# Kernel tuning notes

Hardware: AMD Instinct MI355X
Metric: run time of the kernel (lower is better)

Reference implementation:

```python
import jax, jax.numpy as jnp
import numpy as np
from jax.ops import segment_sum

N_NODES = 100000
N_EDGES = 1600000
IN_DIM, HID_DIM, OUT_DIM = 64, 48, 32


def setup_inputs() -> dict:
    key = jax.random.key(0)
    ks = jax.random.split(key, 4)
    x = jax.random.normal(ks[0], (N_NODES, IN_DIM), dtype=jnp.float32)
    edge_index = jax.random.randint(ks[1], (2, N_EDGES), 0, N_NODES, dtype=jnp.int64)
    W1 = jax.random.normal(ks[2], (IN_DIM, HID_DIM), dtype=jnp.float32) / np.sqrt(IN_DIM)
    b1 = jnp.zeros((HID_DIM,), dtype=jnp.float32)
    W2 = jax.random.normal(ks[3], (HID_DIM, OUT_DIM), dtype=jnp.float32) / np.sqrt(HID_DIM)
    b2 = jnp.zeros((OUT_DIM,), dtype=jnp.float32)
    return {"x": x, "edge_index": edge_index, "W1": W1, "b1": b1, "W2": W2, "b2": b2}


def _gcn_conv(x, W, b, src, dst, deg_inv_sqrt, n_nodes):
    # GCNConv: out = D^{-1/2} (A + I) D^{-1/2} (x W) + b
    h = x @ W                                   # [N, F_out]
    norm = deg_inv_sqrt[src] * deg_inv_sqrt[dst]  # [E+N]
    msg = h[src] * norm[:, None]                # gather + scale
    out = segment_sum(msg, dst, num_segments=n_nodes)  # scatter-add over dst
    return out + b


def reference(x, edge_index, W1, b1, W2, b2):
    n = x.shape[0]
    loop = jnp.arange(n, dtype=edge_index.dtype)
    src = jnp.concatenate([edge_index[0], loop])  # add self-loops (PyG default)
    dst = jnp.concatenate([edge_index[1], loop])
    deg = segment_sum(jnp.ones_like(dst, dtype=x.dtype), dst, num_segments=n)
    deg_inv_sqrt = jnp.where(deg > 0, jax.lax.rsqrt(jnp.maximum(deg, 1.0)), 0.0)
    h = _gcn_conv(x, W1, b1, src, dst, deg_inv_sqrt, n)
    h = jax.nn.relu(h)
    embeddings = _gcn_conv(h, W2, b2, src, dst, deg_inv_sqrt, n)
    return embeddings
```

## Files before the change

### kernel.cpp

```cpp
#include <hip/hip_runtime.h>
#include <hip/hip_fp16.h>


#define NN 100000
#define NE 1600000
#define NPB 128
#define NBUCK ((NN + NPB - 1) / NPB)
#define PBITS 17
#define PMASK ((1 << PBITS) - 1)
#define CHB 3
#define CHS 14
#define NKEY (NPB << CHB)
#define PART_B 512
#define EPT 8
#define PART_G ((NE + PART_B * EPT - 1) / (PART_B * EPT))
#define CAP 4096
#define UN 8

struct alignas(8)  half4 { __half2 lo, hi; };
struct alignas(16) half8 { __half2 a, b, c, d; };

__global__ void k_part(const int* __restrict__ src, const int* __restrict__ dst,
                       int* __restrict__ cursor, int* __restrict__ packed) {
    __shared__ int h[NBUCK];
    __shared__ int base[NBUCK];
    for (int i = threadIdx.x; i < NBUCK; i += blockDim.x) h[i] = 0;
    __syncthreads();
    int ebase = blockIdx.x * (PART_B * EPT);
    for (int k = 0; k < EPT; ++k) {
        int e = ebase + k * PART_B + threadIdx.x;
        if (e < NE) atomicAdd(&h[dst[e] >> 7], 1);
    }
    __syncthreads();
    for (int i = threadIdx.x; i < NBUCK; i += blockDim.x) {
        int c = h[i];
        if (c) base[i] = atomicAdd(&cursor[i], c);
        h[i] = 0;
    }
    __syncthreads();
    for (int k = 0; k < EPT; ++k) {
        int e = ebase + k * PART_B + threadIdx.x;
        if (e < NE) {
            int d = dst[e];
            int b = d >> 7;
            int r = atomicAdd(&h[b], 1);
            packed[(size_t)b * CAP + base[b] + r] = src[e] | ((d & (NPB - 1)) << PBITS);
        }
    }
}

__global__ void k_bsort(const int* __restrict__ packed, const int* __restrict__ cursor,
                        int* __restrict__ srcsort, unsigned int* __restrict__ rowinfo,
                        float* __restrict__ dinv) {
    __shared__ int stage[CAP];
    __shared__ int cnt[NKEY];
    __shared__ int tsum[256];
    int tid = threadIdx.x, b = blockIdx.x;
    int e0 = b * CAP, sz = cursor[b];
    for (int i = tid; i < NKEY; i += 256) cnt[i] = 0;
    __syncthreads();
    for (int i = tid; i < sz; i += 256) {
        int w = packed[e0 + i];
        stage[i] = w;
        int key = ((w >> PBITS) << CHB) | ((w & PMASK) >> CHS);
        atomicAdd(&cnt[key], 1);
    }
    __syncthreads();
    int k0 = tid * 4;
    int c0 = cnt[k0], c1 = cnt[k0 + 1], c2 = cnt[k0 + 2], c3 = cnt[k0 + 3];
    int loc = c0 + c1 + c2 + c3;
    tsum[tid] = loc;
    __syncthreads();
    for (int off = 1; off < 256; off <<= 1) {
        int v = (tid >= off) ? tsum[tid - off] : 0;
        __syncthreads();
        tsum[tid] += v;
        __syncthreads();
    }
    int base = tsum[tid] - loc;
    cnt[k0]     = base;
    cnt[k0 + 1] = base + c0;
    cnt[k0 + 2] = base + c0 + c1;
    cnt[k0 + 3] = base + c0 + c1 + c2;
    __syncthreads();
    if (tid < NPB) {
        int node = b * NPB + tid;
        int rs = cnt[tid << CHB];
        int re = (tid == NPB - 1) ? sz : cnt[(tid + 1) << CHB];
        if (node < NN) {
            rowinfo[node] = ((unsigned int)(e0 + rs) << 10) | (unsigned int)(re - rs);
            dinv[node] = rsqrtf((float)(re - rs + 1));
        }
    }
    __syncthreads();
    for (int i = tid; i < sz; i += 256) {
        int w = stage[i];
        int key = ((w >> PBITS) << CHB) | ((w & PMASK) >> CHS);
        int p = atomicAdd(&cnt[key], 1);
        srcsort[e0 + p] = w & PMASK;
    }
}

template <int K, int NC, int CPT>
__global__ __launch_bounds__(256) void
k_gemm(const float* __restrict__ X, const float* __restrict__ W,
       const float* __restrict__ dinv, __half* __restrict__ Hh, int M) {
    constexpr int CG = NC / CPT;
    constexpr int MT = (256 / CG) * 2;
    constexpr int KF4 = K / 4;
    __shared__ float w[K * NC];
    int tid = threadIdx.x;
    int R0 = blockIdx.x * MT;
    for (int i = tid; i < K * NC; i += 256) w[i] = W[i];
    __syncthreads();

    int tc = tid % CG, tr = tid / CG;
    int r0 = R0 + 2 * tr, r1 = r0 + 1;
    int c0 = tc * CPT;
    bool ok0 = r0 < M, ok1 = r1 < M;
    const float4* X4 = (const float4*)X;
    const float4 z4 = make_float4(0.f, 0.f, 0.f, 0.f);

    float acc[2][CPT];
#pragma unroll
    for (int rr = 0; rr < 2; ++rr)
#pragma unroll
        for (int j = 0; j < CPT; ++j) acc[rr][j] = 0.f;

#pragma unroll 2
    for (int k4 = 0; k4 < KF4; ++k4) {
        float4 xa = ok0 ? X4[(size_t)r0 * KF4 + k4] : z4;
        float4 xb = ok1 ? X4[(size_t)r1 * KF4 + k4] : z4;
        float ar[4] = {xa.x, xa.y, xa.z, xa.w};
        float br[4] = {xb.x, xb.y, xb.z, xb.w};
#pragma unroll
        for (int j = 0; j < 4; ++j) {
            float va = ar[j], vb = br[j];
#pragma unroll
            for (int q = 0; q < CPT / 4; ++q) {
                float4 wv = *(const float4*)&w[(4 * k4 + j) * NC + c0 + 4 * q];
                acc[0][q*4+0] = fmaf(va, wv.x, acc[0][q*4+0]);
                acc[0][q*4+1] = fmaf(va, wv.y, acc[0][q*4+1]);
                acc[0][q*4+2] = fmaf(va, wv.z, acc[0][q*4+2]);
                acc[0][q*4+3] = fmaf(va, wv.w, acc[0][q*4+3]);
                acc[1][q*4+0] = fmaf(vb, wv.x, acc[1][q*4+0]);
                acc[1][q*4+1] = fmaf(vb, wv.y, acc[1][q*4+1]);
                acc[1][q*4+2] = fmaf(vb, wv.z, acc[1][q*4+2]);
                acc[1][q*4+3] = fmaf(vb, wv.w, acc[1][q*4+3]);
            }
        }
    }
#pragma unroll
    for (int rr = 0; rr < 2; ++rr) {
        int gr = r0 + rr;
        if (gr >= M) continue;
        float d = dinv[gr];
#pragma unroll
        for (int q = 0; q < CPT / 4; ++q) {
            __half2 p0 = __floats2half2_rn(acc[rr][q*4+0] * d, acc[rr][q*4+1] * d);
            __half2 p1 = __floats2half2_rn(acc[rr][q*4+2] * d, acc[rr][q*4+3] * d);
            half4 hv; hv.lo = p0; hv.hi = p1;
            *(half4*)(Hh + (size_t)gr * NC + c0 + 4 * q) = hv;
        }
    }
}

__global__ __launch_bounds__(256) void
k_fused48(const __half* __restrict__ Hh, const unsigned int* __restrict__ rowinfo,
          const int* __restrict__ srcsort, const float* __restrict__ dinv,
          const float* __restrict__ b1, const float* __restrict__ W2,
          __half* __restrict__ Hh2) {
    constexpr int ROWS = 128, XS = 49;
    __shared__ float Xs[ROWS * XS];
    __shared__ float w2[48 * 32];
    __shared__ float bb[48];
    int tid = threadIdx.x;
    int R0 = blockIdx.x * ROWS;
    for (int i = tid; i < 48 * 32; i += 256) w2[i] = W2[i];
    if (tid < 48) bb[tid] = b1[tid];
    __syncthreads();

    for (int t = tid; t < ROWS * 6; t += 256) {
        int lr = t / 6, q = t - lr * 6;
        int r = R0 + lr;
        if (r >= NN) continue;
        half8 sv = *(const half8*)(Hh + (size_t)r * 48 + 8 * q);
        float2 f0 = __half22float2(sv.a), f1 = __half22float2(sv.b);
        float2 f2 = __half22float2(sv.c), f3 = __half22float2(sv.d);
        float a0 = f0.x, a1 = f0.y, a2 = f1.x, a3 = f1.y;
        float a4 = f2.x, a5 = f2.y, a6 = f3.x, a7 = f3.y;
        unsigned int rp = rowinfo[r];
        int e0 = rp >> 10, e1 = e0 + (int)(rp & 1023);
        for (int e = e0; e < e1; e += UN) {
            int ss[UN]; float ms[UN];
#pragma unroll
            for (int u = 0; u < UN; ++u) {
                int ee = e + u;
                bool ok = ee < e1;
                ss[u] = srcsort[ok ? ee : e0];
                ms[u] = ok ? 1.f : 0.f;
            }
            half8 vv[UN];
#pragma unroll
            for (int u = 0; u < UN; ++u)
                vv[u] = *(const half8*)(Hh + (size_t)ss[u] * 48 + 8 * q);
#pragma unroll
            for (int u = 0; u < UN; ++u) {
                float2 g0 = __half22float2(vv[u].a), g1 = __half22float2(vv[u].b);
                float2 g2 = __half22float2(vv[u].c), g3 = __half22float2(vv[u].d);
                float m = ms[u];
                a0 = fmaf(g0.x, m, a0); a1 = fmaf(g0.y, m, a1);
                a2 = fmaf(g1.x, m, a2); a3 = fmaf(g1.y, m, a3);
                a4 = fmaf(g2.x, m, a4); a5 = fmaf(g2.y, m, a5);
                a6 = fmaf(g3.x, m, a6); a7 = fmaf(g3.y, m, a7);
            }
        }
        float d = dinv[r];
        float* xr = &Xs[lr * XS + 8 * q];
        const float* bf = &bb[8 * q];
        xr[0] = fmaxf(fmaf(a0, d, bf[0]), 0.f);
        xr[1] = fmaxf(fmaf(a1, d, bf[1]), 0.f);
        xr[2] = fmaxf(fmaf(a2, d, bf[2]), 0.f);
        xr[3] = fmaxf(fmaf(a3, d, bf[3]), 0.f);
        xr[4] = fmaxf(fmaf(a4, d, bf[4]), 0.f);
        xr[5] = fmaxf(fmaf(a5, d, bf[5]), 0.f);
        xr[6] = fmaxf(fmaf(a6, d, bf[6]), 0.f);
        xr[7] = fmaxf(fmaf(a7, d, bf[7]), 0.f);
    }
    __syncthreads();

    int tc = tid & 3, tr = tid >> 2;
    int r0l = 2 * tr, c0 = tc * 8;
    float acc[2][8];
#pragma unroll
    for (int rr = 0; rr < 2; ++rr)
#pragma unroll
        for (int j = 0; j < 8; ++j) acc[rr][j] = 0.f;
#pragma unroll 4
    for (int k = 0; k < 48; ++k) {
        float x0 = Xs[r0l * XS + k];
        float x1 = Xs[(r0l + 1) * XS + k];
        float4 wv0 = *(const float4*)&w2[k * 32 + c0];
        float4 wv1 = *(const float4*)&w2[k * 32 + c0 + 4];
        acc[0][0] = fmaf(x0, wv0.x, acc[0][0]); acc[0][1] = fmaf(x0, wv0.y, acc[0][1]);
        acc[0][2] = fmaf(x0, wv0.z, acc[0][2]); acc[0][3] = fmaf(x0, wv0.w, acc[0][3]);
        acc[0][4] = fmaf(x0, wv1.x, acc[0][4]); acc[0][5] = fmaf(x0, wv1.y, acc[0][5]);
        acc[0][6] = fmaf(x0, wv1.z, acc[0][6]); acc[0][7] = fmaf(x0, wv1.w, acc[0][7]);
        acc[1][0] = fmaf(x1, wv0.x, acc[1][0]); acc[1][1] = fmaf(x1, wv0.y, acc[1][1]);
        acc[1][2] = fmaf(x1, wv0.z, acc[1][2]); acc[1][3] = fmaf(x1, wv0.w, acc[1][3]);
        acc[1][4] = fmaf(x1, wv1.x, acc[1][4]); acc[1][5] = fmaf(x1, wv1.y, acc[1][5]);
        acc[1][6] = fmaf(x1, wv1.z, acc[1][6]); acc[1][7] = fmaf(x1, wv1.w, acc[1][7]);
    }
#pragma unroll
    for (int rr = 0; rr < 2; ++rr) {
        int gr = R0 + r0l + rr;
        if (gr >= NN) continue;
        float d = dinv[gr];
        __half2 p0 = __floats2half2_rn(acc[rr][0] * d, acc[rr][1] * d);
        __half2 p1 = __floats2half2_rn(acc[rr][2] * d, acc[rr][3] * d);
        __half2 p2 = __floats2half2_rn(acc[rr][4] * d, acc[rr][5] * d);
        __half2 p3 = __floats2half2_rn(acc[rr][6] * d, acc[rr][7] * d);
        half8 hv; hv.a = p0; hv.b = p1; hv.c = p2; hv.d = p3;
        *(half8*)(Hh2 + (size_t)gr * 32 + c0) = hv;
    }
}

template <int NC>
__global__ void k_agg(const __half* __restrict__ Hh, const unsigned int* __restrict__ rowinfo,
                      const int* __restrict__ srcsort, const float* __restrict__ dinv,
                      const float* __restrict__ bias, float* __restrict__ out) {
    constexpr int Q = NC / 8;
    int idx = blockIdx.x * blockDim.x + threadIdx.x;
    if (idx >= NN * Q) return;
    int r = idx / Q, q = idx - r * Q;
    half8 sv = *(const half8*)(Hh + (size_t)r * NC + 8 * q);
    float2 f0 = __half22float2(sv.a), f1 = __half22float2(sv.b);
    float2 f2 = __half22float2(sv.c), f3 = __half22float2(sv.d);
    float a0 = f0.x, a1 = f0.y, a2 = f1.x, a3 = f1.y;
    float a4 = f2.x, a5 = f2.y, a6 = f3.x, a7 = f3.y;
    unsigned int rp = rowinfo[r];
    int e0 = rp >> 10, e1 = e0 + (int)(rp & 1023);
    for (int e = e0; e < e1; e += UN) {
        int ss[UN]; float ms[UN];
#pragma unroll
        for (int u = 0; u < UN; ++u) {
            int ee = e + u;
            bool ok = ee < e1;
            ss[u] = srcsort[ok ? ee : e0];
            ms[u] = ok ? 1.f : 0.f;
        }
        half8 vv[UN];
#pragma unroll
        for (int u = 0; u < UN; ++u)
            vv[u] = *(const half8*)(Hh + (size_t)ss[u] * NC + 8 * q);
#pragma unroll
        for (int u = 0; u < UN; ++u) {
            float2 g0 = __half22float2(vv[u].a), g1 = __half22float2(vv[u].b);
            float2 g2 = __half22float2(vv[u].c), g3 = __half22float2(vv[u].d);
            float m = ms[u];
            a0 = fmaf(g0.x, m, a0); a1 = fmaf(g0.y, m, a1);
            a2 = fmaf(g1.x, m, a2); a3 = fmaf(g1.y, m, a3);
            a4 = fmaf(g2.x, m, a4); a5 = fmaf(g2.y, m, a5);
            a6 = fmaf(g3.x, m, a6); a7 = fmaf(g3.y, m, a7);
        }
    }
    float d = dinv[r];
    const float4* b4 = (const float4*)bias;
    float4 bv0 = b4[2 * q], bv1 = b4[2 * q + 1];
    a0 = fmaf(a0, d, bv0.x); a1 = fmaf(a1, d, bv0.y);
    a2 = fmaf(a2, d, bv0.z); a3 = fmaf(a3, d, bv0.w);
    a4 = fmaf(a4, d, bv1.x); a5 = fmaf(a5, d, bv1.y);
    a6 = fmaf(a6, d, bv1.z); a7 = fmaf(a7, d, bv1.w);
    float4* o4 = (float4*)(out + (size_t)r * NC + 8 * q);
    o4[0] = make_float4(a0, a1, a2, a3);
    o4[1] = make_float4(a4, a5, a6, a7);
}

extern "C" void kernel_launch(void* const* d_in, const int* in_sizes, int n_in,
                              void* d_out, int out_size, void* d_ws, size_t ws_size,
                              hipStream_t stream) {
    const float* x  = (const float*)d_in[0];
    const int*   ei = (const int*)d_in[1];
    const float* W1 = (const float*)d_in[2];
    const float* b1 = (const float*)d_in[3];
    const float* W2 = (const float*)d_in[4];
    const float* b2 = (const float*)d_in[5];
    float* out = (float*)d_out;

    const int* src = ei;
    const int* dst = ei + NE;

    char* p = (char*)d_ws;
    auto take = [&](size_t elems) { void* q = p; p += ((elems * 4 + 255) & ~255ull); return q; };
    int*          cursor  = (int*)take(NBUCK);
    unsigned int* rowinfo = (unsigned int*)take(NN);
    float*        dinv    = (float*)take(NN);
    int*          srcsort = (int*)take((size_t)NBUCK * CAP);
    __half*       Hh      = (__half*)take((size_t)NN * 24);
    int*          packed  = (int*)take((size_t)NBUCK * CAP);
    __half*       Hh2     = (__half*)packed;

    const int B = 256;
    const int GB = (NN + 127) / 128;
    hipMemsetAsync(cursor, 0, NBUCK * sizeof(int), stream);
    k_part<<<PART_G, PART_B, 0, stream>>>(src, dst, cursor, packed);
    k_bsort<<<NBUCK, 256, 0, stream>>>(packed, cursor, srcsort, rowinfo, dinv);

    k_gemm<64, 48, 12><<<GB, 256, 0, stream>>>(x, W1, dinv, Hh, NN);
    k_fused48<<<GB, 256, 0, stream>>>(Hh, rowinfo, srcsort, dinv, b1, W2, Hh2);
    k_agg<32><<<(NN * 4 + B - 1) / B, B, 0, stream>>>(Hh2, rowinfo, srcsort, dinv, b2, out);
}
```

Before: 205.9 us.

## Replace two-pass bucket partition with global histogram, scan, and scatter fused into GEMM

Drops the partition-then-local-sort pipeline, which staged packed edges through an intermediate buffer. Edges now go through a global fine-key histogram built with global atomics, a per-bucket scan that turns counts into write offsets, and a direct atomic scatter of source ids into sorted order. The scatter runs as extra blocks inside the layer-1 GEMM launch so both share one dispatch. This removes one full pass over the edges and the packed buffer, at the cost of 1.6M global atomics twice and a larger histogram memset. Edge order within a key is now nondeterministic.

```diff
diff --git a/kernel.cpp b/kernel.cpp
--- a/kernel.cpp
+++ b/kernel.cpp
@@ -11,64 +11,44 @@
 #define CHB 3
 #define CHS 14
 #define NKEY (NPB << CHB)
-#define PART_B 512
-#define EPT 8
-#define PART_G ((NE + PART_B * EPT - 1) / (PART_B * EPT))
 #define CAP 4096
 #define UN 8
+#define EPT 8
+#define SCAT_G ((NE + 256 * EPT - 1) / (256 * EPT))
+#define GB NBUCK
 
 struct alignas(8)  half4 { __half2 lo, hi; };
 struct alignas(16) half8 { __half2 a, b, c, d; };
 
-__global__ void k_part(const int* __restrict__ src, const int* __restrict__ dst,
-                       int* __restrict__ cursor, int* __restrict__ packed) {
-    __shared__ int h[NBUCK];
-    __shared__ int base[NBUCK];
-    for (int i = threadIdx.x; i < NBUCK; i += blockDim.x) h[i] = 0;
-    __syncthreads();
-    int ebase = blockIdx.x * (PART_B * EPT);
-    for (int k = 0; k < EPT; ++k) {
-        int e = ebase + k * PART_B + threadIdx.x;
-        if (e < NE) atomicAdd(&h[dst[e] >> 7], 1);
-    }
-    __syncthreads();
-    for (int i = threadIdx.x; i < NBUCK; i += blockDim.x) {
-        int c = h[i];
-        if (c) base[i] = atomicAdd(&cursor[i], c);
-        h[i] = 0;
-    }
-    __syncthreads();
-    for (int k = 0; k < EPT; ++k) {
-        int e = ebase + k * PART_B + threadIdx.x;
-        if (e < NE) {
-            int d = dst[e];
-            int b = d >> 7;
-            int r = atomicAdd(&h[b], 1);
-            packed[(size_t)b * CAP + base[b] + r] = src[e] | ((d & (NPB - 1)) << PBITS);
-        }
-    }
-}
-
-__global__ void k_bsort(const int* __restrict__ packed, const int* __restrict__ cursor,
-                        int* __restrict__ srcsort, unsigned int* __restrict__ rowinfo,
-                        float* __restrict__ dinv) {
-    __shared__ int stage[CAP];
+__device__ __forceinline__ int edge_key(int s, int d) {
+    return ((d >> 7) << 10) | ((d & (NPB - 1)) << CHB) | (s >> CHS);
+}
+
+__global__ __launch_bounds__(256) void
+k_hist(const int* __restrict__ src, const int* __restrict__ dst,
+       int* __restrict__ hist) {
+    int base = blockIdx.x * (256 * EPT) + threadIdx.x * EPT;
+    if (base >= NE) return;
+    int4 s0 = *(const int4*)(src + base);
+    int4 s1 = *(const int4*)(src + base + 4);
+    int4 d0 = *(const int4*)(dst + base);
+    int4 d1 = *(const int4*)(dst + base + 4);
+    int ss[8] = {s0.x, s0.y, s0.z, s0.w, s1.x, s1.y, s1.z, s1.w};
+    int dd[8] = {d0.x, d0.y, d0.z, d0.w, d1.x, d1.y, d1.z, d1.w};
+#pragma unroll
+    for (int u = 0; u < 8; ++u)
+        atomicAdd(&hist[edge_key(ss[u], dd[u])], 1);
+}
+
+__global__ __launch_bounds__(256) void
+k_scan(int* __restrict__ hist, unsigned int* __restrict__ rowinfo,
+       float* __restrict__ dinv) {
     __shared__ int cnt[NKEY];
     __shared__ int tsum[256];
-    int tid = threadIdx.x, b = blockIdx.x;
-    int e0 = b * CAP, sz = cursor[b];
-    for (int i = tid; i < NKEY; i += 256) cnt[i] = 0;
-    __syncthreads();
-    for (int i = tid; i < sz; i += 256) {
-        int w = packed[e0 + i];
-        stage[i] = w;
-        int key = ((w >> PBITS) << CHB) | ((w & PMASK) >> CHS);
-        atomicAdd(&cnt[key], 1);
-    }
-    __syncthreads();
-    int k0 = tid * 4;
-    int c0 = cnt[k0], c1 = cnt[k0 + 1], c2 = cnt[k0 + 2], c3 = cnt[k0 + 3];
-    int loc = c0 + c1 + c2 + c3;
+    int b = blockIdx.x, tid = threadIdx.x;
+    int k0 = 4 * tid;
+    int4 c = *(const int4*)&hist[(size_t)b * NKEY + k0];
+    int loc = c.x + c.y + c.z + c.w;
     tsum[tid] = loc;
     __syncthreads();
     for (int off = 1; off < 256; off <<= 1) {
@@ -79,45 +59,58 @@
     }
     int base = tsum[tid] - loc;
     cnt[k0]     = base;
-    cnt[k0 + 1] = base + c0;
-    cnt[k0 + 2] = base + c0 + c1;
-    cnt[k0 + 3] = base + c0 + c1 + c2;
-    __syncthreads();
+    cnt[k0 + 1] = base + c.x;
+    cnt[k0 + 2] = base + c.x + c.y;
+    cnt[k0 + 3] = base + c.x + c.y + c.z;
+    __syncthreads();
+    int sz = tsum[255];
     if (tid < NPB) {
         int node = b * NPB + tid;
-        int rs = cnt[tid << CHB];
-        int re = (tid == NPB - 1) ? sz : cnt[(tid + 1) << CHB];
         if (node < NN) {
-            rowinfo[node] = ((unsigned int)(e0 + rs) << 10) | (unsigned int)(re - rs);
+            int rs = cnt[tid << CHB];
+            int re = (tid == NPB - 1) ? sz : cnt[(tid + 1) << CHB];
+            rowinfo[node] = ((unsigned int)(b * CAP + rs) << 10) | (unsigned int)(re - rs);
             dinv[node] = rsqrtf((float)(re - rs + 1));
         }
     }
-    __syncthreads();
-    for (int i = tid; i < sz; i += 256) {
-        int w = stage[i];
-        int key = ((w >> PBITS) << CHB) | ((w & PMASK) >> CHS);
-        int p = atomicAdd(&cnt[key], 1);
-        srcsort[e0 + p] = w & PMASK;
-    }
-}
-
-template <int K, int NC, int CPT>
+    int e0 = b * CAP;
+    int4 o = make_int4(e0 + cnt[k0], e0 + cnt[k0 + 1],
+                       e0 + cnt[k0 + 2], e0 + cnt[k0 + 3]);
+    *(int4*)&hist[(size_t)b * NKEY + k0] = o;
+}
+
 __global__ __launch_bounds__(256) void
-k_gemm(const float* __restrict__ X, const float* __restrict__ W,
-       const float* __restrict__ dinv, __half* __restrict__ Hh, int M) {
-    constexpr int CG = NC / CPT;
-    constexpr int MT = (256 / CG) * 2;
-    constexpr int KF4 = K / 4;
-    __shared__ float w[K * NC];
+k_scatgemm(const int* __restrict__ src, const int* __restrict__ dst,
+           int* __restrict__ hist, int* __restrict__ srcsort,
+           const float* __restrict__ X, const float* __restrict__ W1,
+           const float* __restrict__ dinv, __half* __restrict__ Hh) {
+    __shared__ float w[64 * 48];
     int tid = threadIdx.x;
-    int R0 = blockIdx.x * MT;
-    for (int i = tid; i < K * NC; i += 256) w[i] = W[i];
+    if (blockIdx.x < SCAT_G) {
+        int base = blockIdx.x * (256 * EPT) + tid * EPT;
+        if (base >= NE) return;
+        int4 s0 = *(const int4*)(src + base);
+        int4 s1 = *(const int4*)(src + base + 4);
+        int4 d0 = *(const int4*)(dst + base);
+        int4 d1 = *(const int4*)(dst + base + 4);
+        int ss[8] = {s0.x, s0.y, s0.z, s0.w, s1.x, s1.y, s1.z, s1.w};
+        int dd[8] = {d0.x, d0.y, d0.z, d0.w, d1.x, d1.y, d1.z, d1.w};
+#pragma unroll
+        for (int u = 0; u < 8; ++u) {
+            int p = atomicAdd(&hist[edge_key(ss[u], dd[u])], 1);
+            srcsort[p] = ss[u];
+        }
+        return;
+    }
+    constexpr int NC = 48, CPT = 12, CG = 4, KF4 = 16;
+    int R0 = (blockIdx.x - SCAT_G) * 128;
+    for (int i = tid; i < 64 * 48; i += 256) w[i] = W1[i];
     __syncthreads();
 
     int tc = tid % CG, tr = tid / CG;
     int r0 = R0 + 2 * tr, r1 = r0 + 1;
     int c0 = tc * CPT;
-    bool ok0 = r0 < M, ok1 = r1 < M;
+    bool ok0 = r0 < NN, ok1 = r1 < NN;
     const float4* X4 = (const float4*)X;
     const float4 z4 = make_float4(0.f, 0.f, 0.f, 0.f);
 
@@ -153,7 +146,7 @@
 #pragma unroll
     for (int rr = 0; rr < 2; ++rr) {
         int gr = r0 + rr;
-        if (gr >= M) continue;
+        if (gr >= NN) continue;
         float d = dinv[gr];
 #pragma unroll
         for (int q = 0; q < CPT / 4; ++q) {
@@ -332,21 +325,18 @@
 
     char* p = (char*)d_ws;
     auto take = [&](size_t elems) { void* q = p; p += ((elems * 4 + 255) & ~255ull); return q; };
-    int*          cursor  = (int*)take(NBUCK);
+    int*          hist    = (int*)take((size_t)NBUCK * NKEY);
     unsigned int* rowinfo = (unsigned int*)take(NN);
     float*        dinv    = (float*)take(NN);
     int*          srcsort = (int*)take((size_t)NBUCK * CAP);
     __half*       Hh      = (__half*)take((size_t)NN * 24);
-    int*          packed  = (int*)take((size_t)NBUCK * CAP);
-    __half*       Hh2     = (__half*)packed;
+    __half*       Hh2     = (__half*)take((size_t)NN * 16);
 
     const int B = 256;
-    const int GB = (NN + 127) / 128;
-    hipMemsetAsync(cursor, 0, NBUCK * sizeof(int), stream);
-    k_part<<<PART_G, PART_B, 0, stream>>>(src, dst, cursor, packed);
-    k_bsort<<<NBUCK, 256, 0, stream>>>(packed, cursor, srcsort, rowinfo, dinv);
-
-    k_gemm<64, 48, 12><<<GB, 256, 0, stream>>>(x, W1, dinv, Hh, NN);
+    hipMemsetAsync(hist, 0, (size_t)NBUCK * NKEY * sizeof(int), stream);
+    k_hist<<<SCAT_G, 256, 0, stream>>>(src, dst, hist);
+    k_scan<<<NBUCK, 256, 0, stream>>>(hist, rowinfo, dinv);
+    k_scatgemm<<<SCAT_G + GB, 256, 0, stream>>>(src, dst, hist, srcsort, x, W1, dinv, Hh);
     k_fused48<<<GB, 256, 0, stream>>>(Hh, rowinfo, srcsort, dinv, b1, W2, Hh2);
     k_agg<32><<<(NN * 4 + B - 1) / B, B, 0, stream>>>(Hh2, rowinfo, srcsort, dinv, b2, out);
 }
```

Measured after the change: 374.2 us. +81.7%, slower.

## Fuse edge partitioning with first GEMM and move source-norm scaling into aggregation

Applied to the files above, without the earlier changes.

The first GEMM no longer depends on the degree normalization. Its dinv scaling is dropped and instead applied per edge in the first aggregation, which now gathers dinv[src] for every neighbour. That frees the GEMM to run in the same launch as the edge partition pass, with blocks split by index, removing one kernel launch and letting the GEMM overlap the partition's atomics. The cost is an extra random 4-byte gather per edge in the first aggregation, plus fewer, larger partition blocks (64 edges per thread).

```diff
diff --git a/kernel.cpp b/kernel.cpp
--- a/kernel.cpp
+++ b/kernel.cpp
@@ -11,113 +11,61 @@
 #define CHB 3
 #define CHS 14
 #define NKEY (NPB << CHB)
-#define PART_B 512
-#define EPT 8
-#define PART_G ((NE + PART_B * EPT - 1) / (PART_B * EPT))
 #define CAP 4096
 #define UN 8
+#define PEPT 64
+#define PART_G ((NE + 256 * PEPT - 1) / (256 * PEPT))
+#define GB NBUCK
 
 struct alignas(8)  half4 { __half2 lo, hi; };
 struct alignas(16) half8 { __half2 a, b, c, d; };
 
-__global__ void k_part(const int* __restrict__ src, const int* __restrict__ dst,
-                       int* __restrict__ cursor, int* __restrict__ packed) {
+__global__ __launch_bounds__(256) void
+k_partgemm(const int* __restrict__ src, const int* __restrict__ dst,
+           int* __restrict__ cursor, int* __restrict__ packed,
+           const float* __restrict__ X, const float* __restrict__ W1,
+           __half* __restrict__ Hh) {
     __shared__ int h[NBUCK];
-    __shared__ int base[NBUCK];
-    for (int i = threadIdx.x; i < NBUCK; i += blockDim.x) h[i] = 0;
-    __syncthreads();
-    int ebase = blockIdx.x * (PART_B * EPT);
-    for (int k = 0; k < EPT; ++k) {
-        int e = ebase + k * PART_B + threadIdx.x;
-        if (e < NE) atomicAdd(&h[dst[e] >> 7], 1);
-    }
-    __syncthreads();
-    for (int i = threadIdx.x; i < NBUCK; i += blockDim.x) {
-        int c = h[i];
-        if (c) base[i] = atomicAdd(&cursor[i], c);
-        h[i] = 0;
-    }
-    __syncthreads();
-    for (int k = 0; k < EPT; ++k) {
-        int e = ebase + k * PART_B + threadIdx.x;
-        if (e < NE) {
-            int d = dst[e];
-            int b = d >> 7;
-            int r = atomicAdd(&h[b], 1);
-            packed[(size_t)b * CAP + base[b] + r] = src[e] | ((d & (NPB - 1)) << PBITS);
-        }
-    }
-}
-
-__global__ void k_bsort(const int* __restrict__ packed, const int* __restrict__ cursor,
-                        int* __restrict__ srcsort, unsigned int* __restrict__ rowinfo,
-                        float* __restrict__ dinv) {
-    __shared__ int stage[CAP];
-    __shared__ int cnt[NKEY];
-    __shared__ int tsum[256];
-    int tid = threadIdx.x, b = blockIdx.x;
-    int e0 = b * CAP, sz = cursor[b];
-    for (int i = tid; i < NKEY; i += 256) cnt[i] = 0;
-    __syncthreads();
-    for (int i = tid; i < sz; i += 256) {
-        int w = packed[e0 + i];
-        stage[i] = w;
-        int key = ((w >> PBITS) << CHB) | ((w & PMASK) >> CHS);
-        atomicAdd(&cnt[key], 1);
-    }
-    __syncthreads();
-    int k0 = tid * 4;
-    int c0 = cnt[k0], c1 = cnt[k0 + 1], c2 = cnt[k0 + 2], c3 = cnt[k0 + 3];
-    int loc = c0 + c1 + c2 + c3;
-    tsum[tid] = loc;
-    __syncthreads();
-    for (int off = 1; off < 256; off <<= 1) {
-        int v = (tid >= off) ? tsum[tid - off] : 0;
-        __syncthreads();
-        tsum[tid] += v;
-        __syncthreads();
-    }
-    int base = tsum[tid] - loc;
-    cnt[k0]     = base;
-    cnt[k0 + 1] = base + c0;
-    cnt[k0 + 2] = base + c0 + c1;
-    cnt[k0 + 3] = base + c0 + c1 + c2;
-    __syncthreads();
-    if (tid < NPB) {
-        int node = b * NPB + tid;
-        int rs = cnt[tid << CHB];
-        int re = (tid == NPB - 1) ? sz : cnt[(tid + 1) << CHB];
-        if (node < NN) {
-            rowinfo[node] = ((unsigned int)(e0 + rs) << 10) | (unsigned int)(re - rs);
-            dinv[node] = rsqrtf((float)(re - rs + 1));
-        }
-    }
-    __syncthreads();
-    for (int i = tid; i < sz; i += 256) {
-        int w = stage[i];
-        int key = ((w >> PBITS) << CHB) | ((w & PMASK) >> CHS);
-        int p = atomicAdd(&cnt[key], 1);
-        srcsort[e0 + p] = w & PMASK;
-    }
-}
-
-template <int K, int NC, int CPT>
-__global__ __launch_bounds__(256) void
-k_gemm(const float* __restrict__ X, const float* __restrict__ W,
-       const float* __restrict__ dinv, __half* __restrict__ Hh, int M) {
-    constexpr int CG = NC / CPT;
-    constexpr int MT = (256 / CG) * 2;
-    constexpr int KF4 = K / 4;
-    __shared__ float w[K * NC];
+    __shared__ int base_[NBUCK];
+    __shared__ float w[64 * 48];
     int tid = threadIdx.x;
-    int R0 = blockIdx.x * MT;
-    for (int i = tid; i < K * NC; i += 256) w[i] = W[i];
+
+    if (blockIdx.x < PART_G) {
+        for (int i = tid; i < NBUCK; i += 256) h[i] = 0;
+        __syncthreads();
+        int ebase = blockIdx.x * (256 * PEPT);
+        for (int k = 0; k < PEPT; ++k) {
+            int e = ebase + k * 256 + tid;
+            if (e < NE) atomicAdd(&h[dst[e] >> 7], 1);
+        }
+        __syncthreads();
+        for (int i = tid; i < NBUCK; i += 256) {
+            int c = h[i];
+            if (c) base_[i] = atomicAdd(&cursor[i], c);
+            h[i] = 0;
+        }
+        __syncthreads();
+        for (int k = 0; k < PEPT; ++k) {
+            int e = ebase + k * 256 + tid;
+            if (e < NE) {
+                int d = dst[e];
+                int b = d >> 7;
+                int r = atomicAdd(&h[b], 1);
+                packed[(size_t)b * CAP + base_[b] + r] = src[e] | ((d & (NPB - 1)) << PBITS);
+            }
+        }
+        return;
+    }
+
+    constexpr int NC = 48, CPT = 12, CG = 4, KF4 = 16;
+    int R0 = (blockIdx.x - PART_G) * 128;
+    for (int i = tid; i < 64 * 48; i += 256) w[i] = W1[i];
     __syncthreads();
 
     int tc = tid % CG, tr = tid / CG;
     int r0 = R0 + 2 * tr, r1 = r0 + 1;
     int c0 = tc * CPT;
-    bool ok0 = r0 < M, ok1 = r1 < M;
+    bool ok0 = r0 < NN, ok1 = r1 < NN;
     const float4* X4 = (const float4*)X;
     const float4 z4 = make_float4(0.f, 0.f, 0.f, 0.f);
 
@@ -153,15 +101,66 @@
 #pragma unroll
     for (int rr = 0; rr < 2; ++rr) {
         int gr = r0 + rr;
-        if (gr >= M) continue;
-        float d = dinv[gr];
+        if (gr >= NN) continue;
 #pragma unroll
         for (int q = 0; q < CPT / 4; ++q) {
-            __half2 p0 = __floats2half2_rn(acc[rr][q*4+0] * d, acc[rr][q*4+1] * d);
-            __half2 p1 = __floats2half2_rn(acc[rr][q*4+2] * d, acc[rr][q*4+3] * d);
+            __half2 p0 = __floats2half2_rn(acc[rr][q*4+0], acc[rr][q*4+1]);
+            __half2 p1 = __floats2half2_rn(acc[rr][q*4+2], acc[rr][q*4+3]);
             half4 hv; hv.lo = p0; hv.hi = p1;
             *(half4*)(Hh + (size_t)gr * NC + c0 + 4 * q) = hv;
         }
+    }
+}
+
+__global__ void k_bsort(const int* __restrict__ packed, const int* __restrict__ cursor,
+                        int* __restrict__ srcsort, unsigned int* __restrict__ rowinfo,
+                        float* __restrict__ dinv) {
+    __shared__ int stage[CAP];
+    __shared__ int cnt[NKEY];
+    __shared__ int tsum[256];
+    int tid = threadIdx.x, b = blockIdx.x;
+    int e0 = b * CAP, sz = cursor[b];
+    for (int i = tid; i < NKEY; i += 256) cnt[i] = 0;
+    __syncthreads();
+    for (int i = tid; i < sz; i += 256) {
+        int w = packed[e0 + i];
+        stage[i] = w;
+        int key = ((w >> PBITS) << CHB) | ((w & PMASK) >> CHS);
+        atomicAdd(&cnt[key], 1);
+    }
+    __syncthreads();
+    int k0 = tid * 4;
+    int c0 = cnt[k0], c1 = cnt[k0 + 1], c2 = cnt[k0 + 2], c3 = cnt[k0 + 3];
+    int loc = c0 + c1 + c2 + c3;
+    tsum[tid] = loc;
+    __syncthreads();
+    for (int off = 1; off < 256; off <<= 1) {
+        int v = (tid >= off) ? tsum[tid - off] : 0;
+        __syncthreads();
+        tsum[tid] += v;
+        __syncthreads();
+    }
+    int base = tsum[tid] - loc;
+    cnt[k0]     = base;
+    cnt[k0 + 1] = base + c0;
+    cnt[k0 + 2] = base + c0 + c1;
+    cnt[k0 + 3] = base + c0 + c1 + c2;
+    __syncthreads();
+    if (tid < NPB) {
+        int node = b * NPB + tid;
+        int rs = cnt[tid << CHB];
+        int re = (tid == NPB - 1) ? sz : cnt[(tid + 1) << CHB];
+        if (node < NN) {
+            rowinfo[node] = ((unsigned int)(e0 + rs) << 10) | (unsigned int)(re - rs);
+            dinv[node] = rsqrtf((float)(re - rs + 1));
+        }
+    }
+    __syncthreads();
+    for (int i = tid; i < sz; i += 256) {
+        int w = stage[i];
+        int key = ((w >> PBITS) << CHB) | ((w & PMASK) >> CHS);
+        int p = atomicAdd(&cnt[key], 1);
+        srcsort[e0 + p] = w & PMASK;
     }
 }
 
@@ -184,11 +183,14 @@
         int lr = t / 6, q = t - lr * 6;
         int r = R0 + lr;
         if (r >= NN) continue;
+        float dself = dinv[r];
         half8 sv = *(const half8*)(Hh + (size_t)r * 48 + 8 * q);
         float2 f0 = __half22float2(sv.a), f1 = __half22float2(sv.b);
         float2 f2 = __half22float2(sv.c), f3 = __half22float2(sv.d);
-        float a0 = f0.x, a1 = f0.y, a2 = f1.x, a3 = f1.y;
-        float a4 = f2.x, a5 = f2.y, a6 = f3.x, a7 = f3.y;
+        float a0 = f0.x * dself, a1 = f0.y * dself;
+        float a2 = f1.x * dself, a3 = f1.y * dself;
+        float a4 = f2.x * dself, a5 = f2.y * dself;
+        float a6 = f3.x * dself, a7 = f3.y * dself;
         unsigned int rp = rowinfo[r];
         int e0 = rp >> 10, e1 = e0 + (int)(rp & 1023);
         for (int e = e0; e < e1; e += UN) {
@@ -200,22 +202,24 @@
                 ss[u] = srcsort[ok ? ee : e0];
                 ms[u] = ok ? 1.f : 0.f;
             }
-            half8 vv[UN];
-#pragma unroll
-            for (int u = 0; u < UN; ++u)
+            half8 vv[UN]; float dv[UN];
+#pragma unroll
+            for (int u = 0; u < UN; ++u) {
                 vv[u] = *(const half8*)(Hh + (size_t)ss[u] * 48 + 8 * q);
+                dv[u] = dinv[ss[u]];
+            }
 #pragma unroll
             for (int u = 0; u < UN; ++u) {
                 float2 g0 = __half22float2(vv[u].a), g1 = __half22float2(vv[u].b);
                 float2 g2 = __half22float2(vv[u].c), g3 = __half22float2(vv[u].d);
-                float m = ms[u];
+                float m = ms[u] * dv[u];
                 a0 = fmaf(g0.x, m, a0); a1 = fmaf(g0.y, m, a1);
                 a2 = fmaf(g1.x, m, a2); a3 = fmaf(g1.y, m, a3);
                 a4 = fmaf(g2.x, m, a4); a5 = fmaf(g2.y, m, a5);
                 a6 = fmaf(g3.x, m, a6); a7 = fmaf(g3.y, m, a7);
             }
         }
-        float d = dinv[r];
+        float d = dself;
         float* xr = &Xs[lr * XS + 8 * q];
         const float* bf = &bb[8 * q];
         xr[0] = fmaxf(fmaf(a0, d, bf[0]), 0.f);
@@ -341,12 +345,9 @@
     __half*       Hh2     = (__half*)packed;
 
     const int B = 256;
-    const int GB = (NN + 127) / 128;
     hipMemsetAsync(cursor, 0, NBUCK * sizeof(int), stream);
-    k_part<<<PART_G, PART_B, 0, stream>>>(src, dst, cursor, packed);
+    k_partgemm<<<PART_G + GB, 256, 0, stream>>>(src, dst, cursor, packed, x, W1, Hh);
     k_bsort<<<NBUCK, 256, 0, stream>>>(packed, cursor, srcsort, rowinfo, dinv);
-
-    k_gemm<64, 48, 12><<<GB, 256, 0, stream>>>(x, W1, dinv, Hh, NN);
     k_fused48<<<GB, 256, 0, stream>>>(Hh, rowinfo, srcsort, dinv, b1, W2, Hh2);
     k_agg<32><<<(NN * 4 + B - 1) / B, B, 0, stream>>>(Hh2, rowinfo, srcsort, dinv, b2, out);
 }
```

Result: slower. 231.2 us (+12.3%).
